# Kernel tuning notes

Measured on AMD Instinct MI355X. Metric: run time of the kernel, lower is better.

Reference implementation:

```python
import jax, jax.numpy as jnp
import numpy as np

B, C, F = 8, 2048, 128


def setup_inputs() -> dict:
    key = jax.random.key(0)
    ks = jax.random.split(key, 13)
    features = jax.random.normal(ks[0], (B, C, F), dtype=jnp.float32)
    # sparse-ish boolean adjacency masks over operations
    pred_mask = jax.random.uniform(ks[1], (B, C, C)) < 0.05
    succ_mask = jax.random.uniform(ks[2], (B, C, C)) < 0.05
    same_type_mask = jax.random.uniform(ks[3], (B, C, C)) < 0.10

    def linear(k, fan_in, fan_out):
        kw, kb = jax.random.split(k)
        bound = 1.0 / np.sqrt(fan_in)
        W = jax.random.uniform(kw, (fan_in, fan_out), minval=-bound, maxval=bound, dtype=jnp.float32)
        b = jax.random.uniform(kb, (fan_out,), minval=-bound, maxval=bound, dtype=jnp.float32)
        return W, b

    W_enc, b_enc = linear(ks[4], F, 4 * F)
    W_space, b_space = linear(ks[5], 3 * F, F)
    W_same, b_same = linear(ks[6], 2 * F, F)
    W_mix, b_mix = linear(ks[7], 2 * F, F)
    return {
        "features": features,
        "pred_mask": pred_mask,
        "succ_mask": succ_mask,
        "same_type_mask": same_type_mask,
        "W_enc": W_enc, "b_enc": b_enc,
        "W_space": W_space, "b_space": b_space,
        "W_same": W_same, "b_same": b_same,
        "W_mix": W_mix, "b_mix": b_mix,
    }


def reference(features, pred_mask, succ_mask, same_type_mask,
              W_enc, b_enc, W_space, b_space, W_same, b_same, W_mix, b_mix):
    # encoder: [B,C,F] -> [B,C,4F], split into origin + 3 message features
    enc = features @ W_enc + b_enc
    origin, e_pred, e_succ, e_same = jnp.split(enc, 4, axis=-1)

    def masked_mean(mask, e):
        # original builds (B,C,C,F) broadcast product then sums over 'other';
        # mathematically this is mask @ e with a clamped-degree divisor.
        m = mask.astype(e.dtype)                         # [B,C,C]
        deg = jnp.maximum(m.sum(-1, keepdims=True), 1.0)  # [B,C,1]
        return jnp.einsum('bij,bjf->bif', m, e) / deg

    pred_f = masked_mean(pred_mask, e_pred)
    succ_f = masked_mean(succ_mask, e_succ)
    same_f = masked_mean(same_type_mask, e_same)

    space_mixed = jnp.concatenate([pred_f, origin, succ_f], axis=-1) @ W_space + b_space
    same_mixed = jnp.concatenate([origin, same_f], axis=-1) @ W_same + b_same
    return jnp.concatenate([space_mixed, same_mixed], axis=-1) @ W_mix + b_mix
```

## Files before the change

### kernel.cpp

```cpp
#include <hip/hip_runtime.h>
#include <stdint.h>

typedef unsigned int uint;
typedef unsigned short ushort;
typedef unsigned char uchar;
typedef __attribute__((ext_vector_type(8))) short bf16x8;
typedef __attribute__((ext_vector_type(4))) float f32x4;

__device__ __forceinline__ ushort f2bf(float f) {
  uint u = __builtin_bit_cast(uint, f);
  return (ushort)((u + 0x7FFFu + ((u >> 16) & 1u)) >> 16);
}

__device__ __forceinline__ uint nz4(uint x) {
  uint y = (x & 0x7F7F7F7Fu) + 0x7F7F7F7Fu;
  uint z = (y | x) & 0x80808080u;
  return ((z >> 7) & 1u) | ((z >> 14) & 2u) | ((z >> 21) & 4u) | ((z >> 28) & 8u);
}
__device__ __forceinline__ uint nzd4(uint4 v) {
  return (uint)(v.x != 0u) | ((uint)(v.y != 0u) << 1) |
         ((uint)(v.z != 0u) << 2) | ((uint)(v.w != 0u) << 3);
}
__device__ __forceinline__ bf16x8 bits2bf(uint byte) {
  bf16x8 r;
#pragma unroll
  for (int e = 0; e < 8; ++e)
    r[e] = (short)(ushort)(((byte >> e) & 1u) ? 0x3F80u : 0u);
  return r;
}

__global__ __launch_bounds__(256) void k_detect(
    const uint4* __restrict__ m, int* __restrict__ esz_out) {
  __shared__ int s_ok;
  if (threadIdx.x == 0) s_ok = 1;
  __syncthreads();
  int ok = 1;
#pragma unroll
  for (int i = 0; i < 16; ++i) {
    uint4 v = m[i * 256 + threadIdx.x];
    if (!(v.x <= 1u || v.x == 0x3F800000u)) ok = 0;
    if (!(v.y <= 1u || v.y == 0x3F800000u)) ok = 0;
    if (!(v.z <= 1u || v.z == 0x3F800000u)) ok = 0;
    if (!(v.w <= 1u || v.w == 0x3F800000u)) ok = 0;
  }
  if (!ok) atomicAnd(&s_ok, 0);
  __syncthreads();
  if (threadIdx.x == 0) *esz_out = s_ok ? 4 : 1;
}

__global__ __launch_bounds__(256) void k_prep(
    const float4* __restrict__ fin, ushort* __restrict__ fout,
    const float* __restrict__ We, const float* __restrict__ Ws,
    const float* __restrict__ Wm, const float* __restrict__ Wx,
    ushort* __restrict__ Te, ushort* __restrict__ Ts,
    ushort* __restrict__ Tm, ushort* __restrict__ Tx) {
  const int tid = blockIdx.x * 256 + threadIdx.x;
  for (int i = tid; i < 524288; i += 180224) {
    float4 v = fin[i];
    ushort4 o;
    o.x = f2bf(v.x); o.y = f2bf(v.y); o.z = f2bf(v.z); o.w = f2bf(v.w);
    *(ushort4*)&fout[(size_t)i * 4] = o;
  }
  int i = tid;
  if (i < 65536) { int n = i >> 7, k = i & 127; Te[i] = f2bf(We[k * 512 + n]); return; }
  i -= 65536;
  if (i < 49152) { int n = i / 384, k = i - n * 384; Ts[i] = f2bf(Ws[k * 128 + n]); return; }
  i -= 49152;
  if (i < 32768) { int n = i >> 8, k = i & 255; Tm[i] = f2bf(Wm[k * 128 + n]); return; }
  i -= 32768;
  if (i < 32768) { int n = i >> 8, k = i & 255; Tx[i] = f2bf(Wx[k * 128 + n]); return; }
}

__global__ __launch_bounds__(256) void k_maskpack(
    const void* __restrict__ mp, const void* __restrict__ ms,
    const void* __restrict__ mt, uchar* __restrict__ pk,
    float* __restrict__ invdeg, const int* __restrict__ esz_p) {
  const int t = threadIdx.x;
  const int rg = blockIdx.x;
  const int y = blockIdx.y;
  const int mid = y >> 3, b = y & 7;
  const void* mask = (mid == 0) ? mp : (mid == 1) ? ms : mt;
  const int esz = *esz_p;
  const int rl = t >> 5, seg = t & 31;
  const int r = rg * 8 + rl;
  uint lo, hi;
  if (esz == 1) {
    const uint4* p = (const uint4*)((const uchar*)mask +
                                    ((size_t)b * 2048 + r) * 2048 + seg * 64);
    uint4 v0 = p[0], v1 = p[1], v2 = p[2], v3 = p[3];
    uint q0 = nz4(v0.x) | (nz4(v0.y) << 4) | (nz4(v0.z) << 8) | (nz4(v0.w) << 12);
    uint q1 = nz4(v1.x) | (nz4(v1.y) << 4) | (nz4(v1.z) << 8) | (nz4(v1.w) << 12);
    uint q2 = nz4(v2.x) | (nz4(v2.y) << 4) | (nz4(v2.z) << 8) | (nz4(v2.w) << 12);
    uint q3 = nz4(v3.x) | (nz4(v3.y) << 4) | (nz4(v3.z) << 8) | (nz4(v3.w) << 12);
    lo = q0 | (q1 << 16);
    hi = q2 | (q3 << 16);
  } else {
    const uint4* p = (const uint4*)mask + ((size_t)b * 2048 + r) * 512 + seg * 16;
    uint q[4];
#pragma unroll
    for (int g = 0; g < 4; ++g) {
      uint4 w0 = p[g * 4 + 0], w1 = p[g * 4 + 1];
      uint4 w2 = p[g * 4 + 2], w3 = p[g * 4 + 3];
      q[g] = nzd4(w0) | (nzd4(w1) << 4) | (nzd4(w2) << 8) | (nzd4(w3) << 12);
    }
    lo = q[0] | (q[1] << 16);
    hi = q[2] | (q[3] << 16);
  }
  int cnt = __popc(lo) + __popc(hi);
#pragma unroll
  for (int o = 1; o < 32; o <<= 1) cnt += __shfl_xor(cnt, o);
  if (seg == 0)
    invdeg[((size_t)mid * 8 + b) * 2048 + r] =
        1.0f / (float)(cnt > 0 ? cnt : 1);
  const int mtile = r >> 6, rowin = r & 63;
  uint2 w2v; w2v.x = lo; w2v.y = hi;
  *(uint2*)(pk + (((((size_t)(mid * 8 + b)) * 32 + mtile) * 32 + seg) * 64 +
                  rowin) * 8) = w2v;
}

__global__ __launch_bounds__(256) void k_enc(
    const ushort* __restrict__ featbf, const ushort* __restrict__ WTe,
    const float* __restrict__ bias, ushort* __restrict__ origin,
    ushort* __restrict__ eTt0, ushort* __restrict__ eTt1, ushort* __restrict__ eTt2) {
  __shared__ ushort tr[128 * 64];
  const int t = threadIdx.x;
  const int gm0 = blockIdx.x * 64;
  const int y = blockIdx.y;
  const int lane = t & 63, wave = t >> 6;
  const int m0w = (wave >> 1) * 32, n0w = (wave & 1) * 64;
  const int quad = lane >> 4, lr = lane & 15;
  const ushort* a0p = featbf + (size_t)(gm0 + m0w + lr) * 128 + quad * 8;
  const ushort* a1p = a0p + 16 * 128;
  bf16x8 af0[4], af1[4];
#pragma unroll
  for (int kc = 0; kc < 4; ++kc) {
    af0[kc] = *(const bf16x8*)(a0p + kc * 32);
    af1[kc] = *(const bf16x8*)(a1p + kc * 32);
  }
  f32x4 acc[2][4] = {};
#pragma unroll
  for (int j = 0; j < 4; ++j) {
    const ushort* bp = WTe + (size_t)(y * 128 + n0w + j * 16 + lr) * 128 + quad * 8;
#pragma unroll
    for (int kc = 0; kc < 4; ++kc) {
      bf16x8 bv = *(const bf16x8*)(bp + kc * 32);
      acc[0][j] = __builtin_amdgcn_mfma_f32_16x16x32_bf16(af0[kc], bv, acc[0][j], 0, 0, 0);
      acc[1][j] = __builtin_amdgcn_mfma_f32_16x16x32_bf16(af1[kc], bv, acc[1][j], 0, 0, 0);
    }
  }
  if (y == 0) {
#pragma unroll
    for (int i = 0; i < 2; ++i)
#pragma unroll
      for (int j = 0; j < 4; ++j) {
        int n = n0w + j * 16 + lr;
        float bb = bias[n];
        int mb = gm0 + m0w + i * 16 + quad * 4;
#pragma unroll
        for (int r = 0; r < 4; ++r)
          origin[(size_t)(mb + r) * 128 + n] = f2bf(acc[i][j][r] + bb);
      }
  } else {
#pragma unroll
    for (int i = 0; i < 2; ++i)
#pragma unroll
      for (int j = 0; j < 4; ++j) {
        int n = n0w + j * 16 + lr;
        float bb = bias[y * 128 + n];
        int m_lo = m0w + i * 16 + quad * 4;
        int chunk = m_lo >> 3;
        int byteo = n * 128 + ((chunk ^ (n & 7)) << 4) + (m_lo & 7) * 2;
        ushort4 o;
        o.x = f2bf(acc[i][j][0] + bb);
        o.y = f2bf(acc[i][j][1] + bb);
        o.z = f2bf(acc[i][j][2] + bb);
        o.w = f2bf(acc[i][j][3] + bb);
        *(ushort4*)((char*)tr + byteo) = o;
      }
    __syncthreads();
    ushort* eT = (y == 1) ? eTt0 : (y == 2) ? eTt1 : eTt2;
    const int bb_ = blockIdx.x >> 5, kstep = blockIdx.x & 31;
    uint4* dst = (uint4*)(eT + ((size_t)(bb_ * 32 + kstep)) * 8192);
    const uint4* src = (const uint4*)tr;
#pragma unroll
    for (int ii = 0; ii < 4; ++ii) dst[ii * 256 + t] = src[ii * 256 + t];
  }
}

__global__ __launch_bounds__(256, 3) void k_mm(
    const uchar* __restrict__ pk, const float* __restrict__ invdeg,
    const ushort* __restrict__ B0p, const ushort* __restrict__ B1p,
    const ushort* __restrict__ B2p,
    ushort* __restrict__ P, ushort* __restrict__ S, ushort* __restrict__ T) {
  __shared__ __align__(16) char smem[49152];
  const int t = threadIdx.x;
  const int g = blockIdx.x;
  const int X = g & 7, seq = g >> 3;
  const int pl = seq >> 5, mtile = seq & 31;
  const int panel = pl * 8 + X;
  const int b = panel / 3, mid = panel - b * 3;
  const ushort* Bt = (mid == 0) ? B0p : (mid == 1) ? B1p : B2p;
  ushort* outp = (mid == 0) ? P : (mid == 1) ? S : T;
  const uchar* pkT = pk + ((((size_t)(mid * 8 + b)) * 32 + mtile) * 32) * 512;
  const uchar* BtT = (const uchar*)Bt + ((size_t)b * 32) * 16384;
  const int lane = t & 63, wave = t >> 6;
  const int m0w = (wave >> 1) * 32, n0w = (wave & 1) * 64;
  const int quad = lane >> 4, lr = lane & 15;
  f32x4 acc[2][4] = {};

#define STG_A()                                                               \
  {                                                                           \
    _Pragma("unroll") for (int ii = 0; ii < 4; ++ii)                          \
        __builtin_amdgcn_global_load_lds(                                     \
            (const __attribute__((address_space(1))) uint*)(pkT +             \
                wave * 4096 + ii * 1024 + lane * 16),                         \
            (__attribute__((address_space(3))) uint*)(smem + wave * 4096 +    \
                ii * 1024 + lane * 16),                                       \
            16, 0, 0);                                                        \
  }
#define STG_B(BUF, STEP)                                                      \
  {                                                                           \
    _Pragma("unroll") for (int ii = 0; ii < 4; ++ii)                          \
        __builtin_amdgcn_global_load_lds(                                     \
            (const __attribute__((address_space(1))) uint*)(BtT +             \
                (size_t)(STEP) * 16384 + wave * 4096 + ii * 1024 + lane * 16),\
            (__attribute__((address_space(3))) uint*)(smem + 16384 +          \
                (BUF) * 16384 + wave * 4096 + ii * 1024 + lane * 16),         \
            16, 0, 0);                                                        \
  }
#define CPT(SS, BUF)                                                          \
  {                                                                           \
    const char* Ab = smem;                                                    \
    const char* Bb = smem + 16384 + (BUF) * 16384;                            \
    uint2 wa = *(const uint2*)(Ab + (SS) * 512 + (m0w + lr) * 8);             \
    uint2 wb = *(const uint2*)(Ab + (SS) * 512 + (m0w + 16 + lr) * 8);        \
    _Pragma("unroll") for (int kc = 0; kc < 2; ++kc) {                        \
      uint wax = kc ? wa.y : wa.x;                                            \
      uint wbx = kc ? wb.y : wb.x;                                            \
      bf16x8 a0 = bits2bf((wax >> (quad * 8)) & 0xFFu);                       \
      bf16x8 a1 = bits2bf((wbx >> (quad * 8)) & 0xFFu);                       \
      const int sl = (((kc * 4 + quad) ^ (lr & 7)) << 4);                     \
      bf16x8 b0 = *(const bf16x8*)(Bb + (n0w + lr) * 128 + sl);               \
      bf16x8 b1 = *(const bf16x8*)(Bb + (n0w + 16 + lr) * 128 + sl);          \
      bf16x8 b2 = *(const bf16x8*)(Bb + (n0w + 32 + lr) * 128 + sl);          \
      bf16x8 b3 = *(const bf16x8*)(Bb + (n0w + 48 + lr) * 128 + sl);          \
      __builtin_amdgcn_s_setprio(1);                                          \
      acc[0][0] = __builtin_amdgcn_mfma_f32_16x16x32_bf16(a0, b0, acc[0][0], 0, 0, 0); \
      acc[1][0] = __builtin_amdgcn_mfma_f32_16x16x32_bf16(a1, b0, acc[1][0], 0, 0, 0); \
      acc[0][1] = __builtin_amdgcn_mfma_f32_16x16x32_bf16(a0, b1, acc[0][1], 0, 0, 0); \
      acc[1][1] = __builtin_amdgcn_mfma_f32_16x16x32_bf16(a1, b1, acc[1][1], 0, 0, 0); \
      acc[0][2] = __builtin_amdgcn_mfma_f32_16x16x32_bf16(a0, b2, acc[0][2], 0, 0, 0); \
      acc[1][2] = __builtin_amdgcn_mfma_f32_16x16x32_bf16(a1, b2, acc[1][2], 0, 0, 0); \
      acc[0][3] = __builtin_amdgcn_mfma_f32_16x16x32_bf16(a0, b3, acc[0][3], 0, 0, 0); \
      acc[1][3] = __builtin_amdgcn_mfma_f32_16x16x32_bf16(a1, b3, acc[1][3], 0, 0, 0); \
      __builtin_amdgcn_s_setprio(0);                                          \
    }                                                                         \
  }

  STG_A()
  STG_B(0, 0)
  STG_B(1, 1)
  for (int s = 0; s < 32; ++s) {
    if (s < 31) asm volatile("s_waitcnt vmcnt(4)" ::: "memory");
    else        asm volatile("s_waitcnt vmcnt(0)" ::: "memory");
    __builtin_amdgcn_s_barrier();
    __builtin_amdgcn_sched_barrier(0);
    CPT(s, s & 1)
    asm volatile("" ::: "memory");
    __builtin_amdgcn_s_barrier();
    if (s < 30) STG_B(s & 1, s + 2)
  }
  __builtin_amdgcn_sched_barrier(0);
#undef CPT
#undef STG_B
#undef STG_A

  const size_t rowbase = (size_t)b * 2048 + mtile * 64;
  const float* inv = invdeg + ((size_t)(mid * 8 + b)) * 2048 + mtile * 64;
#pragma unroll
  for (int i = 0; i < 2; ++i)
#pragma unroll
    for (int r = 0; r < 4; ++r) {
      int ml = m0w + i * 16 + quad * 4 + r;
      float iv = inv[ml];
#pragma unroll
      for (int j = 0; j < 4; ++j) {
        int n = n0w + j * 16 + lr;
        outp[(rowbase + ml) * 128 + n] = f2bf(acc[i][j][r] * iv);
      }
    }
}

__device__ __forceinline__ void gemm_body(
    const ushort* __restrict__ A0, const ushort* __restrict__ A1,
    const ushort* __restrict__ A2, const ushort* __restrict__ Bsrc,
    int bstride, int K, const float* __restrict__ bias,
    void* __restrict__ out, int out_f32, int gm0, int t) {
  const int lane = t & 63, wave = t >> 6;
  const int m0w = (wave >> 1) * 32, n0w = (wave & 1) * 64;
  const int quad = lane >> 4, lr = lane & 15;
  const ushort* bbase = Bsrc + (size_t)(n0w + lr) * bstride + quad * 8;
  f32x4 acc[2][4] = {};
  for (int k0 = 0; k0 < K; k0 += 64) {
    const int seg = k0 >> 7;
    const ushort* Ap = (seg == 0) ? A0 : (seg == 1) ? A1 : A2;
    const int ko = k0 & 127;
    const ushort* a0p = Ap + (size_t)(gm0 + m0w + lr) * 128 + ko + quad * 8;
    const ushort* a1p = a0p + 16 * 128;
#pragma unroll
    for (int kc = 0; kc < 2; ++kc) {
      bf16x8 av0 = *(const bf16x8*)(a0p + kc * 32);
      bf16x8 av1 = *(const bf16x8*)(a1p + kc * 32);
      bf16x8 b0 = *(const bf16x8*)(bbase + k0 + kc * 32);
      bf16x8 b1 = *(const bf16x8*)(bbase + (size_t)16 * bstride + k0 + kc * 32);
      bf16x8 b2 = *(const bf16x8*)(bbase + (size_t)32 * bstride + k0 + kc * 32);
      bf16x8 b3 = *(const bf16x8*)(bbase + (size_t)48 * bstride + k0 + kc * 32);
      acc[0][0] = __builtin_amdgcn_mfma_f32_16x16x32_bf16(av0, b0, acc[0][0], 0, 0, 0);
      acc[1][0] = __builtin_amdgcn_mfma_f32_16x16x32_bf16(av1, b0, acc[1][0], 0, 0, 0);
      acc[0][1] = __builtin_amdgcn_mfma_f32_16x16x32_bf16(av0, b1, acc[0][1], 0, 0, 0);
      acc[1][1] = __builtin_amdgcn_mfma_f32_16x16x32_bf16(av1, b1, acc[1][1], 0, 0, 0);
      acc[0][2] = __builtin_amdgcn_mfma_f32_16x16x32_bf16(av0, b2, acc[0][2], 0, 0, 0);
      acc[1][2] = __builtin_amdgcn_mfma_f32_16x16x32_bf16(av1, b2, acc[1][2], 0, 0, 0);
      acc[0][3] = __builtin_amdgcn_mfma_f32_16x16x32_bf16(av0, b3, acc[0][3], 0, 0, 0);
      acc[1][3] = __builtin_amdgcn_mfma_f32_16x16x32_bf16(av1, b3, acc[1][3], 0, 0, 0);
    }
  }
#pragma unroll
  for (int i = 0; i < 2; ++i)
#pragma unroll
    for (int j = 0; j < 4; ++j) {
      const int n = n0w + j * 16 + lr;
      const float bb = bias[n];
      const int mb = gm0 + m0w + i * 16 + quad * 4;
      if (out_f32) {
#pragma unroll
        for (int r = 0; r < 4; ++r)
          ((float*)out)[(size_t)(mb + r) * 128 + n] = acc[i][j][r] + bb;
      } else {
#pragma unroll
        for (int r = 0; r < 4; ++r)
          ((ushort*)out)[(size_t)(mb + r) * 128 + n] = f2bf(acc[i][j][r] + bb);
      }
    }
}

__global__ __launch_bounds__(256) void k_xy(
    const ushort* __restrict__ P, const ushort* __restrict__ origin,
    const ushort* __restrict__ S, const ushort* __restrict__ T,
    const ushort* __restrict__ WTs, const ushort* __restrict__ WTm,
    const float* __restrict__ bs, const float* __restrict__ bm,
    ushort* __restrict__ X, ushort* __restrict__ Y) {
  const int gm0 = blockIdx.x * 64;
  if (blockIdx.y == 0)
    gemm_body(P, origin, S, WTs, 384, 384, bs, X, 0, gm0, threadIdx.x);
  else
    gemm_body(origin, T, nullptr, WTm, 256, 256, bm, Y, 0, gm0, threadIdx.x);
}

__global__ __launch_bounds__(256) void k_mix(
    const ushort* __restrict__ X, const ushort* __restrict__ Y,
    const ushort* __restrict__ WTx, const float* __restrict__ bx,
    float* __restrict__ out) {
  gemm_body(X, Y, nullptr, WTx, 256, 256, bx, out, 1, blockIdx.x * 64, threadIdx.x);
}

extern "C" void kernel_launch(void* const* d_in, const int* in_sizes, int n_in,
                              void* d_out, int out_size, void* d_ws,
                              size_t ws_size, hipStream_t stream) {
  const float* features = (const float*)d_in[0];
  const void* pred = d_in[1];
  const void* succ = d_in[2];
  const void* same = d_in[3];
  const float* W_enc = (const float*)d_in[4];
  const float* b_enc = (const float*)d_in[5];
  const float* W_space = (const float*)d_in[6];
  const float* b_space = (const float*)d_in[7];
  const float* W_same = (const float*)d_in[8];
  const float* b_same = (const float*)d_in[9];
  const float* W_mix = (const float*)d_in[10];
  const float* b_mix = (const float*)d_in[11];

  const size_t M = 16384;
  ushort* w = (ushort*)d_ws;
  ushort* feat_bf = w;  w += M * 128;
  ushort* WT_enc = w;   w += 512 * 128;
  ushort* WT_space = w; w += 128 * 384;
  ushort* WT_same = w;  w += 128 * 256;
  ushort* WT_mix = w;   w += 128 * 256;
  ushort* origin = w;   w += M * 128;
  ushort* eTt0 = w;     w += M * 128;
  ushort* eTt1 = w;     w += M * 128;
  ushort* eTt2 = w;     w += M * 128;
  ushort* P = w;        w += M * 128;
  ushort* S = w;        w += M * 128;
  ushort* T = w;        w += M * 128;
  uchar* pk = (uchar*)w;
  ushort* X = w;
  ushort* Y = w + M * 128;
  w += 6291456;
  float* invdeg = (float*)w;  w += 98304;
  int* esz = (int*)w;

  k_detect<<<1, 256, 0, stream>>>((const uint4*)pred, esz);
  k_prep<<<704, 256, 0, stream>>>((const float4*)features, feat_bf,
                                  W_enc, W_space, W_same, W_mix,
                                  WT_enc, WT_space, WT_same, WT_mix);
  k_maskpack<<<dim3(256, 24), 256, 0, stream>>>(pred, succ, same, pk, invdeg, esz);
  k_enc<<<dim3(256, 4), 256, 0, stream>>>(feat_bf, WT_enc, b_enc,
                                          origin, eTt0, eTt1, eTt2);
  k_mm<<<768, 256, 0, stream>>>(pk, invdeg, eTt0, eTt1, eTt2, P, S, T);
  k_xy<<<dim3(256, 2), 256, 0, stream>>>(P, origin, S, T, WT_space, WT_same,
                                         b_space, b_same, X, Y);
  k_mix<<<256, 256, 0, stream>>>(X, Y, WT_mix, b_mix, (float*)d_out);
}
```

Measured before the change: 490.4 us.

## Fuse prep and maskpack, convert features inside encoder, swizzle packed mask layout

Merges the weight-transpose prep and mask-packing kernels into one launch and drops the separate bf16 feature copy: the encoder now reads fp32 features and converts them to bf16 in registers. The packed mask layout changes to row-major 256-byte rows with an XOR swizzle, and the mm kernel's LDS reads are updated to match. A ballot-based packing path is added for 4-byte masks. This removes one kernel launch and a feature round-trip through memory, at the cost of extra conversion work inside the encoder, which recomputes it for each of its 4 y-blocks.

```diff
diff --git a/kernel.cpp b/kernel.cpp
--- a/kernel.cpp
+++ b/kernel.cpp
@@ -16,10 +16,6 @@
   uint y = (x & 0x7F7F7F7Fu) + 0x7F7F7F7Fu;
   uint z = (y | x) & 0x80808080u;
   return ((z >> 7) & 1u) | ((z >> 14) & 2u) | ((z >> 21) & 4u) | ((z >> 28) & 8u);
-}
-__device__ __forceinline__ uint nzd4(uint4 v) {
-  return (uint)(v.x != 0u) | ((uint)(v.y != 0u) << 1) |
-         ((uint)(v.z != 0u) << 2) | ((uint)(v.w != 0u) << 3);
 }
 __device__ __forceinline__ bf16x8 bits2bf(uint byte) {
   bf16x8 r;
@@ -48,78 +44,90 @@
   if (threadIdx.x == 0) *esz_out = s_ok ? 4 : 1;
 }
 
-__global__ __launch_bounds__(256) void k_prep(
-    const float4* __restrict__ fin, ushort* __restrict__ fout,
+__global__ __launch_bounds__(256) void k_front(
+    const void* __restrict__ mp, const void* __restrict__ ms,
+    const void* __restrict__ mt, uchar* __restrict__ pk,
+    float* __restrict__ invdeg, const int* __restrict__ esz_p,
     const float* __restrict__ We, const float* __restrict__ Ws,
     const float* __restrict__ Wm, const float* __restrict__ Wx,
     ushort* __restrict__ Te, ushort* __restrict__ Ts,
     ushort* __restrict__ Tm, ushort* __restrict__ Tx) {
-  const int tid = blockIdx.x * 256 + threadIdx.x;
-  for (int i = tid; i < 524288; i += 180224) {
-    float4 v = fin[i];
-    ushort4 o;
-    o.x = f2bf(v.x); o.y = f2bf(v.y); o.z = f2bf(v.z); o.w = f2bf(v.w);
-    *(ushort4*)&fout[(size_t)i * 4] = o;
-  }
-  int i = tid;
-  if (i < 65536) { int n = i >> 7, k = i & 127; Te[i] = f2bf(We[k * 512 + n]); return; }
-  i -= 65536;
-  if (i < 49152) { int n = i / 384, k = i - n * 384; Ts[i] = f2bf(Ws[k * 128 + n]); return; }
-  i -= 49152;
-  if (i < 32768) { int n = i >> 8, k = i & 255; Tm[i] = f2bf(Wm[k * 128 + n]); return; }
-  i -= 32768;
-  if (i < 32768) { int n = i >> 8, k = i & 255; Tx[i] = f2bf(Wx[k * 128 + n]); return; }
-}
-
-__global__ __launch_bounds__(256) void k_maskpack(
-    const void* __restrict__ mp, const void* __restrict__ ms,
-    const void* __restrict__ mt, uchar* __restrict__ pk,
-    float* __restrict__ invdeg, const int* __restrict__ esz_p) {
   const int t = threadIdx.x;
-  const int rg = blockIdx.x;
-  const int y = blockIdx.y;
-  const int mid = y >> 3, b = y & 7;
-  const void* mask = (mid == 0) ? mp : (mid == 1) ? ms : mt;
+  if (blockIdx.x >= 1536) {
+    int i = (blockIdx.x - 1536) * 256 + t;
+    if (i < 65536) { int n = i >> 7, k = i & 127; Te[i] = f2bf(We[k * 512 + n]); return; }
+    i -= 65536;
+    if (i < 49152) { int n = i / 384, k = i - n * 384; Ts[i] = f2bf(Ws[k * 128 + n]); return; }
+    i -= 49152;
+    if (i < 32768) { int n = i >> 8, k = i & 255; Tm[i] = f2bf(Wm[k * 128 + n]); return; }
+    i -= 32768;
+    if (i < 32768) { int n = i >> 8, k = i & 255; Tx[i] = f2bf(Wx[k * 128 + n]); return; }
+    return;
+  }
   const int esz = *esz_p;
-  const int rl = t >> 5, seg = t & 31;
-  const int r = rg * 8 + rl;
-  uint lo, hi;
-  if (esz == 1) {
-    const uint4* p = (const uint4*)((const uchar*)mask +
-                                    ((size_t)b * 2048 + r) * 2048 + seg * 64);
-    uint4 v0 = p[0], v1 = p[1], v2 = p[2], v3 = p[3];
-    uint q0 = nz4(v0.x) | (nz4(v0.y) << 4) | (nz4(v0.z) << 8) | (nz4(v0.w) << 12);
-    uint q1 = nz4(v1.x) | (nz4(v1.y) << 4) | (nz4(v1.z) << 8) | (nz4(v1.w) << 12);
-    uint q2 = nz4(v2.x) | (nz4(v2.y) << 4) | (nz4(v2.z) << 8) | (nz4(v2.w) << 12);
-    uint q3 = nz4(v3.x) | (nz4(v3.y) << 4) | (nz4(v3.z) << 8) | (nz4(v3.w) << 12);
-    lo = q0 | (q1 << 16);
-    hi = q2 | (q3 << 16);
+  const int lane = t & 63, wave = t >> 6;
+  if (esz == 4) {
+    const int wgid = blockIdx.x * 4 + wave;
+    for (int rr = wgid; rr < 49152; rr += 6144) {
+      const int mid = rr >> 14, rem = rr & 16383;
+      const int b = rem >> 11, rrow = rem & 2047;
+      const uint* src =
+          (const uint*)((mid == 0) ? mp : (mid == 1) ? ms : mt) +
+          ((size_t)b * 2048 + rrow) * 2048;
+      unsigned long long kept = 0ull;
+#pragma unroll
+      for (int s = 0; s < 32; ++s) {
+        uint v = src[s * 64 + lane];
+        unsigned long long bal = __ballot(v != 0u);
+        if (lane == s) kept = bal;
+      }
+      int cnt = __popcll(kept);
+#pragma unroll
+      for (int o = 1; o < 64; o <<= 1) cnt += __shfl_xor(cnt, o);
+      const int mtile = rrow >> 6, rowin = rrow & 63;
+      uchar* tb = pk + ((((size_t)(mid * 8 + b)) * 32 + mtile)) * 16384;
+      if (lane < 32) {
+        uint2 kv;
+        kv.x = (uint)kept;
+        kv.y = (uint)(kept >> 32);
+        *(uint2*)(tb + rowin * 256 + ((lane ^ (rowin & 31)) << 3)) = kv;
+      }
+      if (lane == 0)
+        invdeg[((size_t)mid * 8 + b) * 2048 + rrow] =
+            1.0f / (float)(cnt > 0 ? cnt : 1);
+    }
   } else {
-    const uint4* p = (const uint4*)mask + ((size_t)b * 2048 + r) * 512 + seg * 16;
-    uint q[4];
-#pragma unroll
-    for (int g = 0; g < 4; ++g) {
-      uint4 w0 = p[g * 4 + 0], w1 = p[g * 4 + 1];
-      uint4 w2 = p[g * 4 + 2], w3 = p[g * 4 + 3];
-      q[g] = nzd4(w0) | (nzd4(w1) << 4) | (nzd4(w2) << 8) | (nzd4(w3) << 12);
-    }
-    lo = q[0] | (q[1] << 16);
-    hi = q[2] | (q[3] << 16);
-  }
-  int cnt = __popc(lo) + __popc(hi);
-#pragma unroll
-  for (int o = 1; o < 32; o <<= 1) cnt += __shfl_xor(cnt, o);
-  if (seg == 0)
-    invdeg[((size_t)mid * 8 + b) * 2048 + r] =
-        1.0f / (float)(cnt > 0 ? cnt : 1);
-  const int mtile = r >> 6, rowin = r & 63;
-  uint2 w2v; w2v.x = lo; w2v.y = hi;
-  *(uint2*)(pk + (((((size_t)(mid * 8 + b)) * 32 + mtile) * 32 + seg) * 64 +
-                  rowin) * 8) = w2v;
+    const int gtid = blockIdx.x * 256 + t;
+    for (int k = 0; k < 4; ++k) {
+      const int u = gtid + k * 393216;
+      const int row = u >> 5, seg = u & 31;
+      const int mid = row >> 14, b = (row >> 11) & 7, rrow = row & 2047;
+      const void* mask = (mid == 0) ? mp : (mid == 1) ? ms : mt;
+      const uint4* p = (const uint4*)((const uchar*)mask +
+                                      ((size_t)b * 2048 + rrow) * 2048 + seg * 64);
+      uint4 v0 = p[0], v1 = p[1], v2 = p[2], v3 = p[3];
+      uint q0 = nz4(v0.x) | (nz4(v0.y) << 4) | (nz4(v0.z) << 8) | (nz4(v0.w) << 12);
+      uint q1 = nz4(v1.x) | (nz4(v1.y) << 4) | (nz4(v1.z) << 8) | (nz4(v1.w) << 12);
+      uint q2 = nz4(v2.x) | (nz4(v2.y) << 4) | (nz4(v2.z) << 8) | (nz4(v2.w) << 12);
+      uint q3 = nz4(v3.x) | (nz4(v3.y) << 4) | (nz4(v3.z) << 8) | (nz4(v3.w) << 12);
+      uint lo = q0 | (q1 << 16);
+      uint hi = q2 | (q3 << 16);
+      int cnt = __popc(lo) + __popc(hi);
+#pragma unroll
+      for (int o = 1; o < 32; o <<= 1) cnt += __shfl_xor(cnt, o);
+      if (seg == 0)
+        invdeg[((size_t)mid * 8 + b) * 2048 + rrow] =
+            1.0f / (float)(cnt > 0 ? cnt : 1);
+      const int mtile = rrow >> 6, rowin = rrow & 63;
+      uint2 w2v; w2v.x = lo; w2v.y = hi;
+      *(uint2*)(pk + ((((size_t)(mid * 8 + b)) * 32 + mtile)) * 16384 +
+                rowin * 256 + ((seg ^ (rowin & 31)) << 3)) = w2v;
+    }
+  }
 }
 
 __global__ __launch_bounds__(256) void k_enc(
-    const ushort* __restrict__ featbf, const ushort* __restrict__ WTe,
+    const float* __restrict__ features, const ushort* __restrict__ WTe,
     const float* __restrict__ bias, ushort* __restrict__ origin,
     ushort* __restrict__ eTt0, ushort* __restrict__ eTt1, ushort* __restrict__ eTt2) {
   __shared__ ushort tr[128 * 64];
@@ -129,13 +137,25 @@
   const int lane = t & 63, wave = t >> 6;
   const int m0w = (wave >> 1) * 32, n0w = (wave & 1) * 64;
   const int quad = lane >> 4, lr = lane & 15;
-  const ushort* a0p = featbf + (size_t)(gm0 + m0w + lr) * 128 + quad * 8;
-  const ushort* a1p = a0p + 16 * 128;
+  const float* a0f = features + (size_t)(gm0 + m0w + lr) * 128 + quad * 8;
+  const float* a1f = a0f + 16 * 128;
   bf16x8 af0[4], af1[4];
 #pragma unroll
   for (int kc = 0; kc < 4; ++kc) {
-    af0[kc] = *(const bf16x8*)(a0p + kc * 32);
-    af1[kc] = *(const bf16x8*)(a1p + kc * 32);
+    float4 x0 = *(const float4*)(a0f + kc * 32);
+    float4 x1 = *(const float4*)(a0f + kc * 32 + 4);
+    float4 y0 = *(const float4*)(a1f + kc * 32);
+    float4 y1 = *(const float4*)(a1f + kc * 32 + 4);
+    bf16x8 a, b;
+    a[0] = (short)f2bf(x0.x); a[1] = (short)f2bf(x0.y);
+    a[2] = (short)f2bf(x0.z); a[3] = (short)f2bf(x0.w);
+    a[4] = (short)f2bf(x1.x); a[5] = (short)f2bf(x1.y);
+    a[6] = (short)f2bf(x1.z); a[7] = (short)f2bf(x1.w);
+    b[0] = (short)f2bf(y0.x); b[1] = (short)f2bf(y0.y);
+    b[2] = (short)f2bf(y0.z); b[3] = (short)f2bf(y0.w);
+    b[4] = (short)f2bf(y1.x); b[5] = (short)f2bf(y1.y);
+    b[6] = (short)f2bf(y1.z); b[7] = (short)f2bf(y1.w);
+    af0[kc] = a; af1[kc] = b;
   }
   f32x4 acc[2][4] = {};
 #pragma unroll
@@ -201,7 +221,7 @@
   const int b = panel / 3, mid = panel - b * 3;
   const ushort* Bt = (mid == 0) ? B0p : (mid == 1) ? B1p : B2p;
   ushort* outp = (mid == 0) ? P : (mid == 1) ? S : T;
-  const uchar* pkT = pk + ((((size_t)(mid * 8 + b)) * 32 + mtile) * 32) * 512;
+  const uchar* pkT = pk + ((((size_t)(mid * 8 + b)) * 32 + mtile)) * 16384;
   const uchar* BtT = (const uchar*)Bt + ((size_t)b * 32) * 16384;
   const int lane = t & 63, wave = t >> 6;
   const int m0w = (wave >> 1) * 32, n0w = (wave & 1) * 64;
@@ -232,8 +252,9 @@
   {                                                                           \
     const char* Ab = smem;                                                    \
     const char* Bb = smem + 16384 + (BUF) * 16384;                            \
-    uint2 wa = *(const uint2*)(Ab + (SS) * 512 + (m0w + lr) * 8);             \
-    uint2 wb = *(const uint2*)(Ab + (SS) * 512 + (m0w + 16 + lr) * 8);        \
+    uint2 wa = *(const uint2*)(Ab + (m0w + lr) * 256 + (((SS) ^ lr) << 3));   \
+    uint2 wb = *(const uint2*)(Ab + (m0w + 16 + lr) * 256 +                   \
+                               (((SS) ^ (16 + lr)) << 3));                    \
     _Pragma("unroll") for (int kc = 0; kc < 2; ++kc) {                        \
       uint wax = kc ? wa.y : wa.x;                                            \
       uint wbx = kc ? wb.y : wb.x;                                            \
@@ -382,7 +403,6 @@
 
   const size_t M = 16384;
   ushort* w = (ushort*)d_ws;
-  ushort* feat_bf = w;  w += M * 128;
   ushort* WT_enc = w;   w += 512 * 128;
   ushort* WT_space = w; w += 128 * 384;
   ushort* WT_same = w;  w += 128 * 256;
@@ -402,11 +422,10 @@
   int* esz = (int*)w;
 
   k_detect<<<1, 256, 0, stream>>>((const uint4*)pred, esz);
-  k_prep<<<704, 256, 0, stream>>>((const float4*)features, feat_bf,
-                                  W_enc, W_space, W_same, W_mix,
-                                  WT_enc, WT_space, WT_same, WT_mix);
-  k_maskpack<<<dim3(256, 24), 256, 0, stream>>>(pred, succ, same, pk, invdeg, esz);
-  k_enc<<<dim3(256, 4), 256, 0, stream>>>(feat_bf, WT_enc, b_enc,
+  k_front<<<2240, 256, 0, stream>>>(pred, succ, same, pk, invdeg, esz,
+                                    W_enc, W_space, W_same, W_mix,
+                                    WT_enc, WT_space, WT_same, WT_mix);
+  k_enc<<<dim3(256, 4), 256, 0, stream>>>(features, WT_enc, b_enc,
                                           origin, eTt0, eTt1, eTt2);
   k_mm<<<768, 256, 0, stream>>>(pk, invdeg, eTt0, eTt1, eTt2, P, S, T);
   k_xy<<<dim3(256, 2), 256, 0, stream>>>(P, origin, S, T, WT_space, WT_same,
```

New measurement: 473.5 us. -3.4%, faster.
